# Kernel tuning notes

Hardware: AMD Instinct MI355X
Metric: run time of the kernel (lower is better)

The kernel has to match this reference:

```python
import jax, jax.numpy as jnp
import numpy as np

V = 32000   # vocab
T = 256     # context len
C = 384     # n_embed
H = 6       # heads
D = 64      # head dim (HEAD_SIZE // NUM_HEADS)
L = 6       # blocks
B = 16      # batch
FF = 4 * C


def setup_inputs() -> dict:
    key = jax.random.key(0)
    ks = jax.random.split(key, 16)
    s = 0.02
    p = {}
    p["x_ids"] = jax.random.randint(ks[0], (B, T), 0, V)
    p["y_ids"] = jax.random.randint(ks[1], (B, T), 0, V)
    p["tok_emb"] = jax.random.normal(ks[2], (V, C), jnp.float32) * s
    p["pos_emb"] = jax.random.normal(ks[3], (T, C), jnp.float32) * s
    p["Wq"] = jax.random.normal(ks[4], (L, H, C, D), jnp.float32) * s
    p["Wk"] = jax.random.normal(ks[5], (L, H, C, D), jnp.float32) * s
    p["Wv"] = jax.random.normal(ks[6], (L, H, C, D), jnp.float32) * s
    p["Wo"] = jax.random.normal(ks[7], (L, H * D, C), jnp.float32) * s
    p["bo"] = jnp.zeros((L, C), jnp.float32)
    p["ln1_s"] = jnp.ones((L, C), jnp.float32)
    p["ln1_b"] = jnp.zeros((L, C), jnp.float32)
    p["ln2_s"] = jnp.ones((L, C), jnp.float32)
    p["ln2_b"] = jnp.zeros((L, C), jnp.float32)
    p["W1"] = jax.random.normal(ks[8], (L, C, FF), jnp.float32) * s
    p["b1"] = jnp.zeros((L, FF), jnp.float32)
    p["W2"] = jax.random.normal(ks[9], (L, FF, C), jnp.float32) * s
    p["b2"] = jnp.zeros((L, C), jnp.float32)
    p["lnf_s"] = jnp.ones((C,), jnp.float32)
    p["lnf_b"] = jnp.zeros((C,), jnp.float32)
    p["Whead"] = jax.random.normal(ks[10], (C, V), jnp.float32) * s
    p["bhead"] = jnp.zeros((V,), jnp.float32)
    return p


def _ln(x, scale, bias, eps=1e-5):
    m = x.mean(-1, keepdims=True)
    v = ((x - m) ** 2).mean(-1, keepdims=True)
    return (x - m) * jax.lax.rsqrt(v + eps) * scale + bias


def reference(x_ids, y_ids, tok_emb, pos_emb, Wq, Wk, Wv, Wo, bo,
              ln1_s, ln1_b, ln2_s, ln2_b, W1, b1, W2, b2,
              lnf_s, lnf_b, Whead, bhead):
    Bq, Tq = x_ids.shape
    x = tok_emb[x_ids] + pos_emb[:Tq]                      # [B,T,C]
    mask = jnp.tril(jnp.ones((Tq, Tq), bool))
    scale = C ** -0.5  # NOTE: original scales by input dim C, not head dim
    for l in range(L):
        h = _ln(x, ln1_s[l], ln1_b[l])
        q = jnp.einsum('btc,hcd->bhtd', h, Wq[l])
        k = jnp.einsum('btc,hcd->bhtd', h, Wk[l])
        v = jnp.einsum('btc,hcd->bhtd', h, Wv[l])
        att = jnp.einsum('bhtd,bhsd->bhts', q, k) * scale
        att = jnp.where(mask, att, -jnp.inf)
        att = jax.nn.softmax(att, axis=-1)
        o = jnp.einsum('bhts,bhsd->bhtd', att, v)
        o = o.transpose(0, 2, 1, 3).reshape(Bq, Tq, H * D)  # concat heads
        x = x + o @ Wo[l] + bo[l]
        h2 = _ln(x, ln2_s[l], ln2_b[l])
        x = x + jax.nn.relu(h2 @ W1[l] + b1[l]) @ W2[l] + b2[l]
    x = _ln(x, lnf_s, lnf_b)
    logits = x @ Whead + bhead                             # [B,T,V]
    logp = jax.nn.log_softmax(logits, axis=-1)
    loss = -jnp.take_along_axis(logp, y_ids[..., None], axis=-1).mean()
    return (logits, loss)
```

## Files before the change

kernel.cpp:

```cpp
#include <hip/hip_runtime.h>

typedef unsigned short u16;
typedef u16   u16x4 __attribute__((ext_vector_type(4)));
typedef u16   u16x8 __attribute__((ext_vector_type(8)));
typedef short s16x8 __attribute__((ext_vector_type(8)));
typedef float f32x4 __attribute__((ext_vector_type(4)));

#define NV 32000
#define NT 256
#define NC 384
#define NH 6
#define ND 64
#define NL 6
#define NB 16
#define NFF 1536
#define NM (NB*NT)
#define QKVSZ (NB*NH*NT*ND)
#define NSLAB (NV/64)

__device__ __forceinline__ u16 f2bf(float f){
    unsigned x = __builtin_bit_cast(unsigned, f);
    x += 0x7fffu + ((x>>16)&1u);
    return (u16)(x>>16);
}

__device__ __forceinline__ void gload_lds16(const u16* g, u16* l){
    __builtin_amdgcn_global_load_lds((const __attribute__((address_space(1))) unsigned int*)g,
                                     (__attribute__((address_space(3))) unsigned int*)l, 16, 0, 0);
}

template<int N> __device__ __forceinline__ void wait_vm(){
    static_assert(N>=0 && N<=4, "add literal");
    if constexpr (N==0) asm volatile("s_waitcnt vmcnt(0)" ::: "memory");
    if constexpr (N==4) asm volatile("s_waitcnt vmcnt(4)" ::: "memory");
}
__device__ __forceinline__ void bar(){
    asm volatile("" ::: "memory");
    __builtin_amdgcn_s_barrier();
    asm volatile("" ::: "memory");
}

__global__ __launch_bounds__(256) void embed_stats(const int* __restrict__ ids,
        const float* __restrict__ tok, const float* __restrict__ pos,
        float* __restrict__ x, u16* __restrict__ xb, float* __restrict__ statp){
    int row  = blockIdx.x*4 + (threadIdx.x>>6);
    int lane = threadIdx.x & 63;
    int t = row & (NT-1);
    const float* tr = tok + (size_t)ids[row]*NC;
    const float* pr = pos + (size_t)t*NC;
    float* xr = x + (size_t)row*NC;
    u16* br = xb + (size_t)row*NC;
    float sum = 0.f, sq = 0.f;
    #pragma unroll
    for (int i=0;i<6;++i){
        int c = lane+64*i;
        float v = tr[c] + pr[c];
        xr[c] = v; br[c] = f2bf(v);
        sum += v; sq += v*v;
    }
    #pragma unroll
    for (int off=1; off<64; off<<=1){ sum += __shfl_xor(sum,off); sq += __shfl_xor(sq,off); }
    if (lane == 0){
        float* pp = statp + (size_t)row*6;
        pp[0]=sum; pp[1]=sq; pp[2]=0.f; pp[3]=0.f; pp[4]=0.f; pp[5]=0.f;
    }
}

struct TDesc {
    const float* in; u16* out;
    int Cc; int nx; int perZ; int obDiv; int oStride; int start;
    long inBatch; long oS1; long oS2; float scale;
    const float* svec; long svecS;
};
struct TPack { TDesc d[7]; };

__global__ __launch_bounds__(256) void tconv_all(TPack p){
    __shared__ float tile[32][33];
    int bid = blockIdx.x;
    int e = 0;
    #pragma unroll
    for (int i=1;i<7;++i) e += (bid >= p.d[i].start) ? 1 : 0;
    TDesc D = p.d[e];
    int local = bid - D.start;
    int bz  = local / D.perZ; int rem = local - bz*D.perZ;
    int cy  = rem / D.nx;     int cx  = rem - cy*D.nx;
    int r0 = cy*32, c0 = cx*32;
    const float* ib = D.in + (size_t)bz*D.inBatch;
    u16* ob = D.out + (size_t)(bz/D.obDiv)*D.oS1 + (size_t)(bz%D.obDiv)*D.oS2;
    const float* sv = D.svec ? D.svec + (size_t)(bz/D.obDiv)*D.svecS : nullptr;
    int tx = threadIdx.x & 31, ty = threadIdx.x >> 5;
    #pragma unroll
    for (int i=0;i<4;++i) tile[ty+8*i][tx] = ib[(size_t)(r0+ty+8*i)*D.Cc + (c0+tx)];
    __syncthreads();
    float f = D.scale * (sv ? sv[r0+tx] : 1.f);
    #pragma unroll
    for (int i=0;i<4;++i) ob[(size_t)(c0+ty+8*i)*D.oStride + (r0+tx)] = f2bf(tile[tx][ty+8*i]*f);
}

struct UVArgs {
    const float *Wq,*Wk,*Wv,*W1,*Wh;
    const float *ln1s,*ln1b,*ln2s,*ln2b,*lnfs,*lnfb;
    float *uvq, *uvf, *uvh; float qscale;
};
__global__ __launch_bounds__(256) void uv_kernel(UVArgs a){
    int gid = blockIdx.x*256 + threadIdx.x;
    const float *W, *s, *b; int kst; float sc = 1.f; float *ou, *ov;
    if (gid < 6*1152){
        int l = gid/1152, n = gid - l*1152;
        int which = n/384, hd = n - which*384, h = hd>>6, d = hd&63;
        const float* Ws = which==0 ? a.Wq : (which==1 ? a.Wk : a.Wv);
        W = Ws + ((size_t)(l*NH+h))*NC*ND + d;
        kst = ND;
        s = a.ln1s + l*NC; b = a.ln1b + l*NC;
        if (which==0) sc = a.qscale;
        ou = a.uvq + (size_t)l*2*1152 + n; ov = ou + 1152;
    } else if (gid < 6*1152 + 6*1536){
        int g = gid - 6*1152; int l = g/1536, f = g - l*1536;
        W = a.W1 + (size_t)l*NC*NFF + f; kst = NFF;
        s = a.ln2s + l*NC; b = a.ln2b + l*NC;
        ou = a.uvf + (size_t)l*2*1536 + f; ov = ou + 1536;
    } else {
        int n = gid - (6*1152 + 6*1536);
        W = a.Wh + n; kst = NV;
        s = a.lnfs; b = a.lnfb;
        ou = a.uvh + n; ov = ou + NV;
    }
    float u = 0.f, v = 0.f;
    for (int k=0;k<NC;++k){ float w = W[(size_t)k*kst]; u += s[k]*w; v += b[k]*w; }
    *ou = u*sc; *ov = v*sc;
}

template<int EPI, int BM, int BN, int LNF>
__global__ __launch_bounds__(256,4) void gemm_bt(
        const u16* __restrict__ A, const u16* __restrict__ Bt,
        const float* __restrict__ bias, float* __restrict__ resid,
        u16* __restrict__ outb,
        const float* __restrict__ statp, const float* __restrict__ uvec,
        const float* __restrict__ vvec, float* __restrict__ stout,
        int M, int N, int K){
    constexpr int WM = BM/2, WN = BN/2, MI = WM/16, NI = WN/16;
    __shared__ u16 As[2*BM*32];
    __shared__ u16 Bs[2*BN*32];
    __shared__ float stM[LNF?BM:1], stR[LNF?BM:1];
    __shared__ float sS[2][16][2], sQ[2][16][2];
    int tid = threadIdx.x;
    int lane = tid & 63, wid = tid >> 6;
    int wm = wid >> 1, wn = wid & 1;
    int l15 = lane & 15, lg = lane >> 4;
    int bx = blockIdx.x, by = blockIdx.y;
    int m0 = by * BM, n0 = bx * BN;

    if constexpr (LNF){
        if (tid < BM){
            const float* pp = statp + (size_t)(m0+tid)*6;
            float s = pp[0]+pp[2]+pp[4];
            float q = pp[1]+pp[3]+pp[5];
            float mu = s*(1.f/NC);
            stM[tid] = mu;
            stR[tid] = rsqrtf(q*(1.f/NC) - mu*mu + 1e-5f);
        }
        __syncthreads();
    }

    f32x4 acc[MI][NI];
    #pragma unroll
    for (int a=0;a<MI;++a)
        #pragma unroll
        for (int b=0;b<NI;++b) acc[a][b] = f32x4{0.f,0.f,0.f,0.f};

    int nk = K >> 6;
    for (int kk = 0; kk < nk; ++kk){
        int k0 = kk << 6;
        #pragma unroll
        for (int h=0;h<2;++h){
            if constexpr (BM >= 64){
                #pragma unroll
                for (int i=0;i<BM/64;++i){
                    int o   = i*4096 + tid*16;
                    int row = o >> 6;
                    int kb  = (o & 63) >> 1;
                    gload_lds16(A + (size_t)(m0+row)*K + (k0+h*32+kb), &As[h*BM*32 + (o>>1)]);
                }
            } else {
                if (tid < BM*4){
                    int o = tid*16;
                    int row = o >> 6;
                    int kb  = (o & 63) >> 1;
                    gload_lds16(A + (size_t)(m0+row)*K + (k0+h*32+kb), &As[h*BM*32 + (o>>1)]);
                }
            }
            #pragma unroll
            for (int i=0;i<BN/64;++i){
                int o   = i*4096 + tid*16;
                int row = o >> 6;
                int kb  = (o & 63) >> 1;
                gload_lds16(Bt + (size_t)(n0+row)*K + (k0+h*32+kb), &Bs[h*BN*32 + (o>>1)]);
            }
        }
        asm volatile("s_waitcnt vmcnt(0)" ::: "memory");
        __syncthreads();
        #pragma unroll
        for (int ks=0;ks<2;++ks){
            s16x8 af[MI];
            #pragma unroll
            for (int mi=0;mi<MI;++mi) af[mi] = *(const s16x8*)&As[ks*BM*32 + (wm*WM+mi*16+l15)*32 + lg*8];
            #pragma unroll
            for (int ni=0;ni<NI;++ni){
                s16x8 bfr = *(const s16x8*)&Bs[ks*BN*32 + (wn*WN+ni*16+l15)*32 + lg*8];
                #pragma unroll
                for (int mi=0;mi<MI;++mi)
                    acc[mi][ni] = __builtin_amdgcn_mfma_f32_16x16x32_bf16(af[mi], bfr, acc[mi][ni], 0,0,0);
            }
        }
        __syncthreads();
    }

    if (EPI == 1){
        float rs[4]={0.f,0.f,0.f,0.f}, rq[4]={0.f,0.f,0.f,0.f};
        #pragma unroll
        for (int ni=0;ni<NI;++ni)
            #pragma unroll
            for (int r=0;r<4;++r){
                int mg = m0 + wm*WM + lg*4 + r;
                int ng = n0 + wn*WN + ni*16 + l15;
                float* pp = resid + (size_t)mg*NC + ng;
                float val = acc[0][ni][r] + bias[ng] + *pp;
                *pp = val;
                outb[(size_t)mg*NC + ng] = f2bf(val);
                rs[r] += val; rq[r] += val*val;
            }
        #pragma unroll
        for (int r=0;r<4;++r){
            rs[r]+=__shfl_xor(rs[r],1); rq[r]+=__shfl_xor(rq[r],1);
            rs[r]+=__shfl_xor(rs[r],2); rq[r]+=__shfl_xor(rq[r],2);
            rs[r]+=__shfl_xor(rs[r],4); rq[r]+=__shfl_xor(rq[r],4);
            rs[r]+=__shfl_xor(rs[r],8); rq[r]+=__shfl_xor(rq[r],8);
            if (l15==0){ sS[wm][lg*4+r][wn]=rs[r]; sQ[wm][lg*4+r][wn]=rq[r]; }
        }
        __syncthreads();
        if (tid < 32){
            int wmi = tid>>4, rr = tid&15;
            float s = sS[wmi][rr][0] + sS[wmi][rr][1];
            float q = sQ[wmi][rr][0] + sQ[wmi][rr][1];
            float* pp = stout + (size_t)(m0+tid)*6 + bx*2;
            pp[0]=s; pp[1]=q;
        }
        return;
    }

    #pragma unroll
    for (int mi=0;mi<MI;++mi){
        #pragma unroll
        for (int ni=0;ni<NI;++ni){
            int ng = n0 + wn*WN + ni*16 + l15;
            if (EPI == 0){
                int which = ng / NC; int hd = ng - which*NC;
                int hh = hd >> 6, d = hd & 63;
                int mgb = m0 + wm*WM + mi*16 + lg*4;
                int bb = mgb >> 8, tt = mgb & (NT-1);
                float uu = uvec[ng], vv0 = vvec[ng];
                if (which == 2){
                    u16x4 v;
                    #pragma unroll
                    for (int r=0;r<4;++r){
                        int lr = wm*WM + mi*16 + lg*4 + r;
                        v[r] = f2bf(stR[lr]*(acc[mi][ni][r] - stM[lr]*uu) + vv0);
                    }
                    *(u16x4*)(outb + (size_t)2*QKVSZ + ((size_t)(bb*NH+hh)*ND + d)*NT + tt) = v;
                } else {
                    #pragma unroll
                    for (int r=0;r<4;++r){
                        int lr = wm*WM + mi*16 + lg*4 + r;
                        float val = stR[lr]*(acc[mi][ni][r] - stM[lr]*uu) + vv0;
                        outb[(size_t)which*QKVSZ + ((size_t)(bb*NH+hh)*NT + tt+r)*ND + d] = f2bf(val);
                    }
                }
            } else {
                float uu = uvec[ng], vv0 = vvec[ng] + bias[ng];
                #pragma unroll
                for (int r=0;r<4;++r){
                    int lr = wm*WM + mi*16 + lg*4 + r;
                    int mg = m0 + lr;
                    float val = stR[lr]*(acc[mi][ni][r] - stM[lr]*uu) + vv0;
                    outb[(size_t)mg*N + ng] = f2bf(fmaxf(val, 0.f));
                }
            }
        }
    }
}

__global__ __launch_bounds__(256,4) void gemm_head(
        const u16* __restrict__ A, const u16* __restrict__ Bt,
        const float* __restrict__ bias,
        const float* __restrict__ statp, const float* __restrict__ uvec,
        const float* __restrict__ vvec,
        float* __restrict__ outf, float* __restrict__ lpart,
        int M, int N, int K){
    constexpr int BM=128, BN=128, WM=64, WN=64, MI=4, NI=4;
    __shared__ u16 As[2][BM*32];
    __shared__ u16 Bs[2][BN*32];
    __shared__ float stM[BM], stR[BM];
    int tid = threadIdx.x;
    int lane = tid & 63, wid = tid >> 6;
    int wm = wid >> 1, wn = wid & 1;
    int l15 = lane & 15, lg = lane >> 4;
    int nwg = gridDim.x*gridDim.y;
    int orig = blockIdx.y*gridDim.x + blockIdx.x;
    int swz = (orig&7)*(nwg>>3) + (orig>>3);
    int by = swz & 31;
    int bx = swz >> 5;
    int m0 = by * BM, n0 = bx * BN;

    if (tid < BM){
        const float* pp = statp + (size_t)(m0+tid)*6;
        float s = pp[0]+pp[2]+pp[4];
        float q = pp[1]+pp[3]+pp[5];
        float mu = s*(1.f/NC);
        stM[tid] = mu;
        stR[tid] = rsqrtf(q*(1.f/NC) - mu*mu + 1e-5f);
    }
    __syncthreads();

    f32x4 acc[MI][NI];
    #pragma unroll
    for (int a=0;a<MI;++a)
        #pragma unroll
        for (int b=0;b<NI;++b) acc[a][b] = f32x4{0.f,0.f,0.f,0.f};

    auto STAGE = [&](int kt, int buf){
        int k0 = kt << 5;
        #pragma unroll
        for (int i=0;i<2;++i){
            int o   = i*4096 + tid*16;
            int row = o >> 6;
            int kb  = (o & 63) >> 1;
            gload_lds16(A + (size_t)(m0+row)*K + (k0+kb), &As[buf][o>>1]);
        }
        #pragma unroll
        for (int i=0;i<2;++i){
            int o   = i*4096 + tid*16;
            int row = o >> 6;
            int kb  = (o & 63) >> 1;
            gload_lds16(Bt + (size_t)(n0+row)*K + (k0+kb), &Bs[buf][o>>1]);
        }
    };

    int nk = K >> 5;
    STAGE(0, 0);
    for (int t = 0; t < nk; ++t){
        int buf = t & 1;
        if (t+1 < nk){ STAGE(t+1, buf^1); wait_vm<4>(); }
        else         { wait_vm<0>(); }
        bar();
        s16x8 af[MI];
        #pragma unroll
        for (int mi=0;mi<MI;++mi) af[mi] = *(const s16x8*)&As[buf][(wm*WM+mi*16+l15)*32 + lg*8];
        #pragma unroll
        for (int ni=0;ni<NI;++ni){
            s16x8 bfr = *(const s16x8*)&Bs[buf][(wn*WN+ni*16+l15)*32 + lg*8];
            #pragma unroll
            for (int mi=0;mi<MI;++mi)
                acc[mi][ni] = __builtin_amdgcn_mfma_f32_16x16x32_bf16(af[mi], bfr, acc[mi][ni], 0,0,0);
        }
        bar();
    }

    float es[MI][4];
    #pragma unroll
    for (int mi=0;mi<MI;++mi)
        #pragma unroll
        for (int r=0;r<4;++r) es[mi][r] = 0.f;
    #pragma unroll
    for (int mi=0;mi<MI;++mi)
        #pragma unroll
        for (int ni=0;ni<NI;++ni){
            int ng = n0 + wn*WN + ni*16 + l15;
            float uu = uvec[ng], vv0 = vvec[ng] + bias[ng];
            #pragma unroll
            for (int r=0;r<4;++r){
                int lr = wm*WM + mi*16 + lg*4 + r;
                int mg = m0 + lr;
                float val = stR[lr]*(acc[mi][ni][r] - stM[lr]*uu) + vv0;
                outf[(size_t)mg*N + ng] = val;
                es[mi][r] += __expf(val);
            }
        }
    #pragma unroll
    for (int mi=0;mi<MI;++mi)
        #pragma unroll
        for (int r=0;r<4;++r){
            float s = es[mi][r];
            s += __shfl_xor(s,1); s += __shfl_xor(s,2);
            s += __shfl_xor(s,4); s += __shfl_xor(s,8);
            if (l15 == 0){
                int mg = m0 + wm*WM + mi*16 + lg*4 + r;
                lpart[(size_t)mg*NSLAB + bx*2 + wn] = s;
            }
        }
}

__global__ __launch_bounds__(256,2) void attn_kernel(const u16* __restrict__ qkv, u16* __restrict__ o){
    int blk = blockIdx.x;
    int qt = blk & 3, bh = blk >> 2;
    int b = bh / NH, h = bh - b*NH;
    int tid = threadIdx.x, lane = tid & 63, w = tid >> 6;
    int l15 = lane & 15, lg = lane >> 4;
    __shared__ u16 Ks[256*72];
    __shared__ u16 Vt[64*264];
    __shared__ u16 Ps[4][16*72];
    const u16* qb = qkv + (size_t)bh*NT*ND;
    const u16* kb = qkv + QKVSZ + (size_t)bh*NT*ND;
    const u16* vb = qkv + (size_t)2*QKVSZ + (size_t)bh*ND*NT;
    int nit = (qt+1)*2;
    for (int it=0; it<nit; ++it){
        int e0 = (it*256 + tid)*8;
        int row = e0 >> 6, col = e0 & 63;
        *(u16x8*)&Ks[row*72+col] = *(const u16x8*)(kb + e0);
    }
    for (int kt2=0; kt2<=qt; ++kt2){
        #pragma unroll
        for (int it=0; it<2; ++it){
            int e0 = (it*256 + tid)*8;
            int d = e0 >> 6, t = e0 & 63;
            *(u16x8*)&Vt[d*264 + kt2*64 + t] = *(const u16x8*)(vb + (size_t)d*NT + kt2*64 + t);
        }
    }
    const u16* qrow = qb + (size_t)(qt*64 + w*16 + l15)*ND;
    s16x8 qf[2];
    qf[0] = *(const s16x8*)(qrow + lg*8);
    qf[1] = *(const s16x8*)(qrow + 32 + lg*8);
    __syncthreads();

    f32x4 oacc[4]; float l_[4];
    #pragma unroll
    for (int c=0;c<4;++c){ oacc[c]=f32x4{0.f,0.f,0.f,0.f}; l_[c]=0.f; }
    u16* Pw = &Ps[w][0];

    for (int kt=0; kt<=qt; ++kt){
        f32x4 sacc[4];
        #pragma unroll
        for (int c=0;c<4;++c) sacc[c]=f32x4{0.f,0.f,0.f,0.f};
        #pragma unroll
        for (int ks=0;ks<2;++ks){
            s16x8 kf[4];
            #pragma unroll
            for (int ni=0;ni<4;++ni)
                kf[ni] = *(const s16x8*)&Ks[(kt*64+ni*16+l15)*72 + ks*32 + lg*8];
            #pragma unroll
            for (int ni=0;ni<4;++ni)
                sacc[ni] = __builtin_amdgcn_mfma_f32_16x16x32_bf16(qf[ks], kf[ni], sacc[ni], 0,0,0);
        }
        if (kt == qt){
            #pragma unroll
            for (int ni=0;ni<4;++ni)
                #pragma unroll
                for (int r=0;r<4;++r)
                    if (ni*16+l15 > w*16+lg*4+r) sacc[ni][r] = -1e30f;
        }
        #pragma unroll
        for (int r=0;r<4;++r){
            float rs = 0.f;
            #pragma unroll
            for (int ni=0;ni<4;++ni){
                float p = __expf(sacc[ni][r]);
                sacc[ni][r] = p;
                rs += p;
                Pw[(lg*4+r)*72 + ni*16 + l15] = f2bf(p);
            }
            rs += __shfl_xor(rs,1); rs += __shfl_xor(rs,2);
            rs += __shfl_xor(rs,4); rs += __shfl_xor(rs,8);
            l_[r] += rs;
        }
        #pragma unroll
        for (int ks=0;ks<2;++ks){
            s16x8 pf, vf[4];
            pf = *(const s16x8*)&Pw[l15*72 + ks*32 + lg*8];
            #pragma unroll
            for (int ni=0;ni<4;++ni)
                vf[ni] = *(const s16x8*)&Vt[(ni*16+l15)*264 + kt*64 + ks*32 + lg*8];
            #pragma unroll
            for (int ni=0;ni<4;++ni)
                oacc[ni] = __builtin_amdgcn_mfma_f32_16x16x32_bf16(pf, vf[ni], oacc[ni], 0,0,0);
        }
    }
    #pragma unroll
    for (int ni=0;ni<4;++ni)
        #pragma unroll
        for (int r=0;r<4;++r){
            int t = qt*64 + w*16 + lg*4 + r;
            int d = ni*16 + l15;
            o[((size_t)(b*NT + t))*NC + h*ND + d] = f2bf(oacc[ni][r] / l_[r]);
        }
}

__global__ __launch_bounds__(256) void loss_rows2(const float* __restrict__ lpart,
        const float* __restrict__ logits, const int* __restrict__ y, float* __restrict__ rowloss){
    int row  = blockIdx.x*4 + (threadIdx.x>>6);
    int lane = threadIdx.x & 63;
    const float* pr = lpart + (size_t)row*NSLAB;
    float s = 0.f;
    for (int i = lane; i < NSLAB; i += 64) s += pr[i];
    #pragma unroll
    for (int off=1; off<64; off<<=1) s += __shfl_xor(s, off);
    if (lane==0)
        rowloss[row] = logf(s) - logits[(size_t)row*NV + y[row]];
}

__global__ __launch_bounds__(256) void loss_final(const float* __restrict__ rowloss, float* __restrict__ out){
    int tid = threadIdx.x;
    float s = 0.f;
    for (int i = tid; i < NM; i += 256) s += rowloss[i];
    #pragma unroll
    for (int off=1; off<64; off<<=1) s += __shfl_xor(s, off);
    __shared__ float ss[4];
    if ((tid&63)==0) ss[tid>>6]=s;
    __syncthreads();
    if (tid==0) out[0] = (ss[0]+ss[1]+ss[2]+ss[3]) * (1.f/NM);
}

extern "C" void kernel_launch(void* const* d_in, const int* in_sizes, int n_in,
                              void* d_out, int out_size, void* d_ws, size_t ws_size,
                              hipStream_t stream){
    const int*   x_ids = (const int*)  d_in[0];
    const int*   y_ids = (const int*)  d_in[1];
    const float* tok   = (const float*)d_in[2];
    const float* pos   = (const float*)d_in[3];
    const float* Wq    = (const float*)d_in[4];
    const float* Wk    = (const float*)d_in[5];
    const float* Wv    = (const float*)d_in[6];
    const float* Wo    = (const float*)d_in[7];
    const float* bo    = (const float*)d_in[8];
    const float* ln1s  = (const float*)d_in[9];
    const float* ln1b  = (const float*)d_in[10];
    const float* ln2s  = (const float*)d_in[11];
    const float* ln2b  = (const float*)d_in[12];
    const float* W1    = (const float*)d_in[13];
    const float* b1    = (const float*)d_in[14];
    const float* W2    = (const float*)d_in[15];
    const float* b2    = (const float*)d_in[16];
    const float* lnfs  = (const float*)d_in[17];
    const float* lnfb  = (const float*)d_in[18];
    const float* Wh    = (const float*)d_in[19];
    const float* bh    = (const float*)d_in[20];

    float* logits = (float*)d_out;
    float* lossp  = logits + (size_t)NM*NV;

    char* ws = (char*)d_ws;
    auto alloc = [&](size_t bytes)->char*{ char* p = ws; ws += (bytes + 255) & ~(size_t)255; return p; };
    float* xf    = (float*)alloc((size_t)NM*NC*4);
    u16*   xb    = (u16*)  alloc((size_t)NM*NC*2);
    float* statp = (float*)alloc((size_t)NM*6*4);
    u16*   qkvb  = (u16*)  alloc((size_t)3*QKVSZ*2);
    u16*   obf   = (u16*)  alloc((size_t)NM*NC*2);
    u16*   f1bf  = (u16*)  alloc((size_t)NM*NFF*2);
    u16*   qkvw  = (u16*)  alloc((size_t)NL*1152*NC*2);
    u16*   wot   = (u16*)  alloc((size_t)NL*NC*NC*2);
    u16*   w1t   = (u16*)  alloc((size_t)NL*NFF*NC*2);
    u16*   w2t   = (u16*)  alloc((size_t)NL*NC*NFF*2);
    u16*   wht   = (u16*)  alloc((size_t)NV*NC*2);
    float* uvq   = (float*)alloc((size_t)NL*2*1152*4);
    float* uvf   = (float*)alloc((size_t)NL*2*1536*4);
    float* uvh   = (float*)alloc((size_t)2*NV*4);
    float* part  = (float*)alloc((size_t)NM*4);
    float* lpart = (float*)qkvb;

    const float qscale = 0.051031036307982884f;

    TPack tp;
    tp.d[0] = {Wq, qkvw + 0*(NC*NC), ND,  2,  24, NH, NC, 0,     (long)NC*ND, (long)1152*NC, (long)ND*NC, qscale, ln1s, NC};
    tp.d[1] = {Wk, qkvw + 1*(NC*NC), ND,  2,  24, NH, NC, 864,   (long)NC*ND, (long)1152*NC, (long)ND*NC, 1.f,    ln1s, NC};
    tp.d[2] = {Wv, qkvw + 2*(NC*NC), ND,  2,  24, NH, NC, 1728,  (long)NC*ND, (long)1152*NC, (long)ND*NC, 1.f,    ln1s, NC};
    tp.d[3] = {Wo, wot,              NC, 12, 144, 1,  NC, 2592,  (long)NC*NC, (long)NC*NC,   0,           1.f,    nullptr, 0};
    tp.d[4] = {W1, w1t,             NFF, 48, 576, 1,  NC, 3456,  (long)NC*NFF,(long)NFF*NC,  0,           1.f,    ln2s, NC};
    tp.d[5] = {W2, w2t,              NC, 12, 576, 1, NFF, 6912,  (long)NFF*NC,(long)NC*NFF,  0,           1.f,    nullptr, 0};
    tp.d[6] = {Wh, wht,              NV,1000,12000,1, NC, 10368, 0,           0,             0,           1.f,    lnfs, 0};
    tconv_all<<<22368,256,0,stream>>>(tp);

    UVArgs ua = {Wq, Wk, Wv, W1, Wh, ln1s, ln1b, ln2s, ln2b, lnfs, lnfb, uvq, uvf, uvh, qscale};
    uv_kernel<<<(6*1152 + 6*1536 + NV)/256, 256, 0, stream>>>(ua);

    embed_stats<<<NM/4,256,0,stream>>>(x_ids, tok, pos, xf, xb, statp);
    for (int l = 0; l < NL; ++l){
        gemm_bt<0,64,128,1><<<dim3(1152/128, NM/64),256,0,stream>>>(
                xb, qkvw + (size_t)l*1152*NC, nullptr, nullptr, qkvb,
                statp, uvq + (size_t)l*2*1152, uvq + (size_t)l*2*1152 + 1152, nullptr,
                NM, 1152, NC);
        attn_kernel<<<NB*NH*4,256,0,stream>>>(qkvb, obf);
        gemm_bt<1,32,128,0><<<dim3(NC/128, NM/32),256,0,stream>>>(
                obf, wot + (size_t)l*NC*NC, bo + l*NC, xf, xb,
                nullptr, nullptr, nullptr, statp, NM, NC, NC);
        gemm_bt<2,64,128,1><<<dim3(NFF/128, NM/64),256,0,stream>>>(
                xb, w1t + (size_t)l*NFF*NC, b1 + l*NFF, nullptr, f1bf,
                statp, uvf + (size_t)l*2*1536, uvf + (size_t)l*2*1536 + 1536, nullptr,
                NM, NFF, NC);
        gemm_bt<1,32,128,0><<<dim3(NC/128, NM/32),256,0,stream>>>(
                f1bf, w2t + (size_t)l*NC*NFF, b2 + l*NC, xf, xb,
                nullptr, nullptr, nullptr, statp, NM, NC, NFF);
    }
    gemm_head<<<dim3(NV/128, NM/128),256,0,stream>>>(xb, wht, bh,
            statp, uvh, uvh + NV, logits, lpart, NM, NV, NC);
    loss_rows2<<<NM/4,256,0,stream>>>(lpart, logits, y_ids, part);
    loss_final<<<1,256,0,stream>>>(part, lossp);
}
```

Before: 750.3 us.

## Shrink head GEMM tile to 128x64 and drop double buffering for occupancy

The LM-head GEMM tile goes from 128x128 to 128x64, which doubles the grid and halves the per-wave N fragments. Its LDS double buffering becomes a single buffer with a full vmcnt(0) wait and __syncthreads each k-step, and launch bounds rise to 8 waves per SIMD. The aim is more resident workgroups to hide latency through occupancy rather than software pipelining. In exchange the A tile is reloaded twice as often, and loads are no longer overlapped with MFMA work inside a block. The slab count for loss partials is doubled to match the narrower N tile.

```diff
diff --git a/kernel.cpp b/kernel.cpp
--- a/kernel.cpp
+++ b/kernel.cpp
@@ -16,7 +16,7 @@
 #define NFF 1536
 #define NM (NB*NT)
 #define QKVSZ (NB*NH*NT*ND)
-#define NSLAB (NV/64)
+#define NSLAB (NV/32)
 
 __device__ __forceinline__ u16 f2bf(float f){
     unsigned x = __builtin_bit_cast(unsigned, f);
@@ -27,17 +27,6 @@
 __device__ __forceinline__ void gload_lds16(const u16* g, u16* l){
     __builtin_amdgcn_global_load_lds((const __attribute__((address_space(1))) unsigned int*)g,
                                      (__attribute__((address_space(3))) unsigned int*)l, 16, 0, 0);
-}
-
-template<int N> __device__ __forceinline__ void wait_vm(){
-    static_assert(N>=0 && N<=4, "add literal");
-    if constexpr (N==0) asm volatile("s_waitcnt vmcnt(0)" ::: "memory");
-    if constexpr (N==4) asm volatile("s_waitcnt vmcnt(4)" ::: "memory");
-}
-__device__ __forceinline__ void bar(){
-    asm volatile("" ::: "memory");
-    __builtin_amdgcn_s_barrier();
-    asm volatile("" ::: "memory");
 }
 
 __global__ __launch_bounds__(256) void embed_stats(const int* __restrict__ ids,
@@ -289,16 +278,16 @@
     }
 }
 
-__global__ __launch_bounds__(256,4) void gemm_head(
+__global__ __launch_bounds__(256,8) void gemm_head(
         const u16* __restrict__ A, const u16* __restrict__ Bt,
         const float* __restrict__ bias,
         const float* __restrict__ statp, const float* __restrict__ uvec,
         const float* __restrict__ vvec,
         float* __restrict__ outf, float* __restrict__ lpart,
         int M, int N, int K){
-    constexpr int BM=128, BN=128, WM=64, WN=64, MI=4, NI=4;
-    __shared__ u16 As[2][BM*32];
-    __shared__ u16 Bs[2][BN*32];
+    constexpr int BM=128, BN=64, WM=64, WN=32, MI=4, NI=2;
+    __shared__ u16 As[BM*32];
+    __shared__ u16 Bs[BN*32];
     __shared__ float stM[BM], stR[BM];
     int tid = threadIdx.x;
     int lane = tid & 63, wid = tid >> 6;
@@ -327,42 +316,35 @@
         #pragma unroll
         for (int b=0;b<NI;++b) acc[a][b] = f32x4{0.f,0.f,0.f,0.f};
 
-    auto STAGE = [&](int kt, int buf){
-        int k0 = kt << 5;
+    int nk = K >> 5;
+    for (int kk = 0; kk < nk; ++kk){
+        int k0 = kk << 5;
         #pragma unroll
         for (int i=0;i<2;++i){
             int o   = i*4096 + tid*16;
             int row = o >> 6;
             int kb  = (o & 63) >> 1;
-            gload_lds16(A + (size_t)(m0+row)*K + (k0+kb), &As[buf][o>>1]);
-        }
-        #pragma unroll
-        for (int i=0;i<2;++i){
-            int o   = i*4096 + tid*16;
+            gload_lds16(A + (size_t)(m0+row)*K + (k0+kb), &As[o>>1]);
+        }
+        {
+            int o   = tid*16;
             int row = o >> 6;
             int kb  = (o & 63) >> 1;
-            gload_lds16(Bt + (size_t)(n0+row)*K + (k0+kb), &Bs[buf][o>>1]);
-        }
-    };
-
-    int nk = K >> 5;
-    STAGE(0, 0);
-    for (int t = 0; t < nk; ++t){
-        int buf = t & 1;
-        if (t+1 < nk){ STAGE(t+1, buf^1); wait_vm<4>(); }
-        else         { wait_vm<0>(); }
-        bar();
+            gload_lds16(Bt + (size_t)(n0+row)*K + (k0+kb), &Bs[o>>1]);
+        }
+        asm volatile("s_waitcnt vmcnt(0)" ::: "memory");
+        __syncthreads();
         s16x8 af[MI];
         #pragma unroll
-        for (int mi=0;mi<MI;++mi) af[mi] = *(const s16x8*)&As[buf][(wm*WM+mi*16+l15)*32 + lg*8];
+        for (int mi=0;mi<MI;++mi) af[mi] = *(const s16x8*)&As[(wm*WM+mi*16+l15)*32 + lg*8];
         #pragma unroll
         for (int ni=0;ni<NI;++ni){
-            s16x8 bfr = *(const s16x8*)&Bs[buf][(wn*WN+ni*16+l15)*32 + lg*8];
+            s16x8 bfr = *(const s16x8*)&Bs[(wn*WN+ni*16+l15)*32 + lg*8];
             #pragma unroll
             for (int mi=0;mi<MI;++mi)
                 acc[mi][ni] = __builtin_amdgcn_mfma_f32_16x16x32_bf16(af[mi], bfr, acc[mi][ni], 0,0,0);
         }
-        bar();
+        __syncthreads();
     }
 
     float es[MI][4];
@@ -598,7 +580,7 @@
                 f1bf, w2t + (size_t)l*NC*NFF, b2 + l*NC, xf, xb,
                 nullptr, nullptr, nullptr, statp, NM, NC, NFF);
     }
-    gemm_head<<<dim3(NV/128, NM/128),256,0,stream>>>(xb, wht, bh,
+    gemm_head<<<dim3(NV/64, NM/128),256,0,stream>>>(xb, wht, bh,
             statp, uvh, uvh + NV, logits, lpart, NM, NV, NC);
     loss_rows2<<<NM/4,256,0,stream>>>(lpart, logits, y_ids, part);
     loss_final<<<1,256,0,stream>>>(part, lossp);
```

Result: slower. 805.5 us (+7.4%).
